# Performance work log

Measured on AMD Instinct MI355X. Metric: run time of the kernel, lower is better.

Reference implementation:

```python
import jax, jax.numpy as jnp
import numpy as np

NEG_INF = -1e30

def _pool_unpool(x, k):
    # x: [B, C, H, W]. Non-overlapping max pool with window k (floor-mode,
    # matching torch MaxPool2d default), then MaxUnpool: scatter the pooled max
    # back to its argmax location within each window, zeros elsewhere.
    B, C, H, W = x.shape
    Hc, Wc = (H // k) * k, (W // k) * k  # cropped region covered by windows
    xc = x[:, :, :Hc, :Wc]
    # reshape into windows: [B, C, H/k, k, W/k, k] -> [B, C, H/k, W/k, k*k]
    xw = xc.reshape(B, C, Hc // k, k, Wc // k, k).transpose(0, 1, 2, 4, 3, 5)
    xw = xw.reshape(B, C, Hc // k, Wc // k, k * k)
    mx = jnp.max(xw, axis=-1, keepdims=True)
    am = jnp.argmax(xw, axis=-1)  # first max index, matches torch tie-breaking
    onehot = (jnp.arange(k * k) == am[..., None])
    yw = jnp.where(onehot, mx, jnp.zeros_like(mx))
    yc = yw.reshape(B, C, Hc // k, Wc // k, k, k).transpose(0, 1, 2, 4, 3, 5)
    yc = yc.reshape(B, C, Hc, Wc)
    # output_size=size in torch unpool -> pad uncovered border with zeros
    return jnp.pad(yc, ((0, 0), (0, 0), (0, H - Hc), (0, W - Wc)))

def setup_inputs() -> dict:
    key = jax.random.key(0)
    x = jax.random.uniform(key, (16, 1, 1080, 1920), dtype=jnp.float32)
    return {"x": x}

def reference(x):
    k = 3
    x = _pool_unpool(x, k)
    x = _pool_unpool(x, k + 2)
    x = _pool_unpool(x, k + 3)
    return x
```

## Files before the change

kernel.cpp:

```cpp
#include <hip/hip_runtime.h>
#include <stdint.h>


#define IMG_H 1080
#define IMG_W 1920

template <int K>
__device__ __forceinline__ void stage(float (&v)[30], int rc, int h) {
    constexpr int NH = 30 / K;
    const int g = rc / K;
    const int myrr = rc - g * K;
    const int srcbase = (h << 5) + g * K;
#pragma unroll
    for (int j = 0; j < NH; ++j) {
        float hm = v[j * K];
#pragma unroll
        for (int c = 1; c < K; ++c) hm = fmaxf(hm, v[j * K + c]);
        float m = -1.0f;
        int fr = -1;
#pragma unroll
        for (int rr = 0; rr < K; ++rr) {
            const float tv = __shfl(hm, srcbase + rr, 64);
            if (tv > m) { m = tv; fr = rr; }
        }
        const bool rowwin = (fr == myrr);
        bool seen = false;
#pragma unroll
        for (int c = 0; c < K; ++c) {
            const bool eq = (v[j * K + c] == m);
            if (!(rowwin && eq && !seen)) v[j * K + c] = 0.0f;
            seen = seen || eq;
        }
    }
}

__global__ __launch_bounds__(256) void pooling_nms_kernel(
    const float* __restrict__ x, float* __restrict__ out) {
    const int t = threadIdx.x;
    const int w = t >> 6;
    const int lane = t & 63;
    const int h = lane >> 5;
    const int r = lane & 31;
    const int rc = (r < 30) ? r : 29;

    const int col0 = blockIdx.x * 240 + w * 60 + h * 30;
    const size_t base = (size_t)blockIdx.z * (IMG_H * (size_t)IMG_W) +
                        (size_t)(blockIdx.y * 30 + rc) * IMG_W + col0;
    const float* src = x + base;
    float* dst = out + base;

    float v[30];
    if (r < 30) {
        if (h == 0) {
#pragma unroll
            for (int q = 0; q < 7; ++q)
                *reinterpret_cast<float4*>(&v[4 * q]) =
                    *reinterpret_cast<const float4*>(src + 4 * q);
            *reinterpret_cast<float2*>(&v[28]) =
                *reinterpret_cast<const float2*>(src + 28);
        } else {
            *reinterpret_cast<float2*>(&v[0]) =
                *reinterpret_cast<const float2*>(src);
#pragma unroll
            for (int q = 0; q < 7; ++q)
                *reinterpret_cast<float4*>(&v[2 + 4 * q]) =
                    *reinterpret_cast<const float4*>(src + 2 + 4 * q);
        }
    }

    stage<3>(v, rc, h);
    stage<5>(v, rc, h);
    stage<6>(v, rc, h);

    if (r < 30) {
        if (h == 0) {
#pragma unroll
            for (int q = 0; q < 7; ++q)
                *reinterpret_cast<float4*>(dst + 4 * q) =
                    *reinterpret_cast<const float4*>(&v[4 * q]);
            *reinterpret_cast<float2*>(dst + 28) =
                *reinterpret_cast<const float2*>(&v[28]);
        } else {
            *reinterpret_cast<float2*>(dst) =
                *reinterpret_cast<const float2*>(&v[0]);
#pragma unroll
            for (int q = 0; q < 7; ++q)
                *reinterpret_cast<float4*>(dst + 2 + 4 * q) =
                    *reinterpret_cast<const float4*>(&v[2 + 4 * q]);
        }
    }
}

extern "C" void kernel_launch(void* const* d_in, const int* in_sizes, int n_in,
                              void* d_out, int out_size, void* d_ws, size_t ws_size,
                              hipStream_t stream) {
    const float* x = (const float*)d_in[0];
    float* out = (float*)d_out;
    dim3 grid(IMG_W / 240, IMG_H / 30, 16);
    pooling_nms_kernel<<<grid, 256, 0, stream>>>(x, out);
}
```

Before: 288.7 us.

## Transpose thread mapping to column-per-lane with coalesced scalar loads and mask-based argmax

Each lane now owns one image column and holds 30 rows in registers, replacing the previous layout where each lane owned a row segment of 30 columns and loaded it with float4 vectors. Loads and stores become scalar but coalesced across the 60 active lanes of each row. The horizontal window reduction now uses shuffles of column maxima, and the first-max tie-break in row-major order is resolved with shuffled equality bitmasks. Launch bounds also request 6 blocks per CU. The intent is better memory coalescing and fewer serial compare-select chains, at the cost of more shuffles (two rounds per window) and scalar memory instructions.

After: 241.7 us. 16.3% less time.

```diff
diff --git a/kernel.cpp b/kernel.cpp
--- a/kernel.cpp
+++ b/kernel.cpp
@@ -6,88 +6,67 @@
 #define IMG_W 1920
 
 template <int K>
-__device__ __forceinline__ void stage(float (&v)[30], int rc, int h) {
-    constexpr int NH = 30 / K;
-    const int g = rc / K;
-    const int myrr = rc - g * K;
-    const int srcbase = (h << 5) + g * K;
+__device__ __forceinline__ void stage(float (&v)[30], int cg, int cc) {
+    constexpr int NW = 30 / K;
 #pragma unroll
-    for (int j = 0; j < NH; ++j) {
-        float hm = v[j * K];
+    for (int j = 0; j < NW; ++j) {
+        float vm = v[j * K];
 #pragma unroll
-        for (int c = 1; c < K; ++c) hm = fmaxf(hm, v[j * K + c]);
-        float m = -1.0f;
-        int fr = -1;
+        for (int rr = 1; rr < K; ++rr) vm = fmaxf(vm, v[j * K + rr]);
+        float M = vm;
 #pragma unroll
-        for (int rr = 0; rr < K; ++rr) {
-            const float tv = __shfl(hm, srcbase + rr, 64);
-            if (tv > m) { m = tv; fr = rr; }
+        for (int q = 0; q < K; ++q) M = fmaxf(M, __shfl(vm, cg + q, 64));
+        unsigned mask = 0u;
+#pragma unroll
+        for (int rr = 0; rr < K; ++rr)
+            mask |= (v[j * K + rr] == M) ? (1u << rr) : 0u;
+        unsigned comb = 0u, pre = 0u;
+#pragma unroll
+        for (int q = 0; q < K; ++q) {
+            const unsigned mq = (unsigned)__shfl((int)mask, cg + q, 64);
+            comb |= mq;
+            pre |= (q < cc) ? mq : 0u;
         }
-        const bool rowwin = (fr == myrr);
-        bool seen = false;
+        const int R = __ffs(comb) - 1;
+        const bool win = ((mask >> R) & 1u) != 0u && ((pre >> R) & 1u) == 0u;
 #pragma unroll
-        for (int c = 0; c < K; ++c) {
-            const bool eq = (v[j * K + c] == m);
-            if (!(rowwin && eq && !seen)) v[j * K + c] = 0.0f;
-            seen = seen || eq;
-        }
+        for (int rr = 0; rr < K; ++rr)
+            v[j * K + rr] = (win && rr == R) ? M : 0.0f;
     }
 }
 
-__global__ __launch_bounds__(256) void pooling_nms_kernel(
+__global__ __launch_bounds__(256, 6) void pooling_nms_kernel(
     const float* __restrict__ x, float* __restrict__ out) {
     const int t = threadIdx.x;
     const int w = t >> 6;
     const int lane = t & 63;
-    const int h = lane >> 5;
-    const int r = lane & 31;
-    const int rc = (r < 30) ? r : 29;
-
-    const int col0 = blockIdx.x * 240 + w * 60 + h * 30;
+    const int c = (lane < 60) ? lane : 59;
+    const int col0 = blockIdx.x * 240 + w * 60;
     const size_t base = (size_t)blockIdx.z * (IMG_H * (size_t)IMG_W) +
-                        (size_t)(blockIdx.y * 30 + rc) * IMG_W + col0;
+                        (size_t)(blockIdx.y * 30) * IMG_W + col0 + c;
     const float* src = x + base;
     float* dst = out + base;
 
     float v[30];
-    if (r < 30) {
-        if (h == 0) {
 #pragma unroll
-            for (int q = 0; q < 7; ++q)
-                *reinterpret_cast<float4*>(&v[4 * q]) =
-                    *reinterpret_cast<const float4*>(src + 4 * q);
-            *reinterpret_cast<float2*>(&v[28]) =
-                *reinterpret_cast<const float2*>(src + 28);
-        } else {
-            *reinterpret_cast<float2*>(&v[0]) =
-                *reinterpret_cast<const float2*>(src);
-#pragma unroll
-            for (int q = 0; q < 7; ++q)
-                *reinterpret_cast<float4*>(&v[2 + 4 * q]) =
-                    *reinterpret_cast<const float4*>(src + 2 + 4 * q);
-        }
+    for (int r = 0; r < 30; ++r) v[r] = src[(size_t)r * IMG_W];
+
+    {
+        const int cg = (c / 3) * 3;
+        stage<3>(v, cg, c - cg);
+    }
+    {
+        const int cg = (c / 5) * 5;
+        stage<5>(v, cg, c - cg);
+    }
+    {
+        const int cg = (c / 6) * 6;
+        stage<6>(v, cg, c - cg);
     }
 
-    stage<3>(v, rc, h);
-    stage<5>(v, rc, h);
-    stage<6>(v, rc, h);
-
-    if (r < 30) {
-        if (h == 0) {
+    if (lane < 60) {
 #pragma unroll
-            for (int q = 0; q < 7; ++q)
-                *reinterpret_cast<float4*>(dst + 4 * q) =
-                    *reinterpret_cast<const float4*>(&v[4 * q]);
-            *reinterpret_cast<float2*>(dst + 28) =
-                *reinterpret_cast<const float2*>(&v[28]);
-        } else {
-            *reinterpret_cast<float2*>(dst) =
-                *reinterpret_cast<const float2*>(&v[0]);
-#pragma unroll
-            for (int q = 0; q < 7; ++q)
-                *reinterpret_cast<float4*>(dst + 2 + 4 * q) =
-                    *reinterpret_cast<const float4*>(&v[2 + 4 * q]);
-        }
+        for (int r = 0; r < 30; ++r) dst[(size_t)r * IMG_W] = v[r];
     }
 }
 
```
